# Optimization experiments

Hardware: AMD Instinct MI355X
Metric: run time of the kernel (lower is better)

## Reference

```python
import jax, jax.numpy as jnp
import numpy as np

INF = 10000000000000.0
HEADS = 12
HEAD_SIZE = 64

def _rope_tables(seqlen, dim):
    inv_freq = 1.0 / (10000.0 ** (jnp.arange(0, dim, 2, dtype=jnp.float32) / dim))
    t = jnp.arange(seqlen, dtype=jnp.float32)
    freqs = t[:, None] * inv_freq[None, :]            # [S, d/2]
    # unsqueeze_dim=-2 -> [S, 1, d/2] to broadcast over heads
    return jnp.sin(freqs)[:, None, :], jnp.cos(freqs)[:, None, :]

def _apply_rope(t, sin, cos):
    # t: [B, S, H, D]; sin/cos: [S, 1, D/2]
    t1, t2 = t[..., 0::2], t[..., 1::2]
    out = jnp.stack([t1 * cos - t2 * sin, t1 * sin + t2 * cos], axis=-1)
    return out.reshape(t.shape)

def setup_inputs() -> dict:
    key = jax.random.key(0)
    k1, k2 = jax.random.split(key)
    B, S, Hd = 32, 512, 1024
    x = jax.random.normal(k1, (B, S, Hd), dtype=jnp.float32)
    W = jax.random.normal(k2, (Hd, HEADS * 2 * HEAD_SIZE), dtype=jnp.float32) * (1.0 / np.sqrt(Hd))
    b = jnp.zeros((HEADS * 2 * HEAD_SIZE,), dtype=jnp.float32)
    attention_mask = jnp.ones((B, S), dtype=jnp.int32)
    return {"x": x, "W": W, "b": b, "attention_mask": attention_mask}

def reference(x, W, b, attention_mask):
    B, S, _ = x.shape
    proj = x @ W + b                                   # [B, S, H*2*D]
    proj = proj.reshape(B, S, HEADS, 2, HEAD_SIZE)
    qw, kw = proj[..., 0, :], proj[..., 1, :]          # [B, S, H, D]
    sin, cos = _rope_tables(S, HEAD_SIZE)
    qw = _apply_rope(qw, sin, cos)
    kw = _apply_rope(kw, sin, cos)
    logits = jnp.einsum('bmhd,bnhd->bhmn', qw, kw)     # [B, H, S, S]
    am = attention_mask.astype(logits.dtype)
    pad_mask = 1.0 - am[:, None, None, :] * am[:, None, :, None]
    logits = logits - pad_mask * INF
    idx = jnp.arange(S)
    tril = (idx[:, None] > idx[None, :]).astype(logits.dtype)  # strictly lower triangle
    logits = logits - tril * INF
    return logits / (HEAD_SIZE ** 0.5)
```

## Files before the change

kernel.cpp:

```cpp
#include <hip/hip_runtime.h>
#include <hip/hip_bf16.h>
#include <cstdint>

#define HEADS 12
#define HEAD_SIZE 64
#define SEQ 512
#define HD 1024
#define NPROJ 1536
#define INF_VAL 1e13f

typedef __attribute__((ext_vector_type(8))) __bf16 bf16x8;
typedef __attribute__((ext_vector_type(4))) float f32x4;

__device__ __forceinline__ unsigned short f2bf(float f) {
    unsigned u = __float_as_uint(f);
    u += 0x7fffu + ((u >> 16) & 1u);
    return (unsigned short)(u >> 16);
}

__device__ __forceinline__ void gl_lds16(const unsigned short* g, unsigned short* l) {
    __builtin_amdgcn_global_load_lds(
        (const __attribute__((address_space(1))) unsigned int*)g,
        (__attribute__((address_space(3))) unsigned int*)l, 16, 0, 0);
}

__global__ void __launch_bounds__(256) convert_x(const float* __restrict__ x,
                                                 unsigned short* __restrict__ xb) {
    const int i = blockIdx.x * 256 + threadIdx.x;
    const float4* src = (const float4*)x;
    float4 v0 = src[i * 2 + 0];
    float4 v1 = src[i * 2 + 1];
    uint4 p;
    p.x = f2bf(v0.x) | ((unsigned)f2bf(v0.y) << 16);
    p.y = f2bf(v0.z) | ((unsigned)f2bf(v0.w) << 16);
    p.z = f2bf(v1.x) | ((unsigned)f2bf(v1.y) << 16);
    p.w = f2bf(v1.z) | ((unsigned)f2bf(v1.w) << 16);
    ((uint4*)xb)[i] = p;
}

__global__ void __launch_bounds__(256) transpose_cast_w(const float* __restrict__ W,
                                                        unsigned short* __restrict__ Wt) {
    __shared__ unsigned short tile[64][65];
    const int bx = blockIdx.x;
    const int k0 = (bx & 15) * 64;
    const int n0 = (bx >> 4) * 64;
    const int t = threadIdx.x;
    const int tr = t >> 4;
    const int tc = (t & 15) * 4;
#pragma unroll
    for (int i = 0; i < 4; ++i) {
        int kk = tr + i * 16;
        float4 v = *(const float4*)&W[(size_t)(k0 + kk) * NPROJ + n0 + tc];
        tile[kk][tc + 0] = f2bf(v.x);
        tile[kk][tc + 1] = f2bf(v.y);
        tile[kk][tc + 2] = f2bf(v.z);
        tile[kk][tc + 3] = f2bf(v.w);
    }
    __syncthreads();
#pragma unroll
    for (int i = 0; i < 4; ++i) {
        int nn = tr + i * 16;
        ushort4 o;
        o.x = tile[tc + 0][nn];
        o.y = tile[tc + 1][nn];
        o.z = tile[tc + 2][nn];
        o.w = tile[tc + 3][nn];
        *(ushort4*)&Wt[(size_t)(n0 + nn) * HD + k0 + tc] = o;
    }
}

__global__ void __launch_bounds__(256) gemm1_rope(const unsigned short* __restrict__ xb,
                                                  const unsigned short* __restrict__ Wt,
                                                  const float* __restrict__ bias,
                                                  unsigned short* __restrict__ qws,
                                                  unsigned short* __restrict__ kws) {
    __shared__ __align__(16) char smem[32768];
    unsigned short* Alds = (unsigned short*)smem;
    unsigned short* Blds = (unsigned short*)(smem + 8192);

    const int bx = blockIdx.x;
    const int tile_m = bx / HEADS;
    const int h = bx - tile_m * HEADS;
    const int m0 = tile_m * 128;
    const int n0 = h * 128;

    const int t = threadIdx.x;
    const int w = t >> 6;
    const int lane = t & 63;
    const int wm = w >> 1;
    const int wn = w & 1;
    const int c16 = lane & 15;
    const int quad = lane >> 4;

    const int row0 = w * 32 + (lane >> 2);
    const int celem = (lane & 3) * 8;
    const unsigned short* ga0 = xb + (size_t)(m0 + row0) * HD + celem;
    const unsigned short* ga1 = xb + (size_t)(m0 + row0 + 16) * HD + celem;
    const unsigned short* gb0 = Wt + (size_t)(n0 + row0) * HD + celem;
    const unsigned short* gb1 = Wt + (size_t)(n0 + row0 + 16) * HD + celem;
    unsigned short* la0 = Alds + row0 * 32 + celem;
    unsigned short* la1 = Alds + (row0 + 16) * 32 + celem;
    unsigned short* lb0 = Blds + row0 * 32 + celem;
    unsigned short* lb1 = Blds + (row0 + 16) * 32 + celem;

    f32x4 acc[4][4];
#pragma unroll
    for (int i = 0; i < 4; ++i)
#pragma unroll
        for (int j = 0; j < 4; ++j) acc[i][j] = (f32x4){0.f, 0.f, 0.f, 0.f};

    for (int kt = 0; kt < HD; kt += 32) {
        gl_lds16(ga0 + kt, la0);
        gl_lds16(ga1 + kt, la1);
        gl_lds16(gb0 + kt, lb0);
        gl_lds16(gb1 + kt, lb1);
        __syncthreads();

        bf16x8 af[4], bfr[4];
#pragma unroll
        for (int mi = 0; mi < 4; ++mi)
            af[mi] = *(const bf16x8*)((char*)Alds + (wm * 64 + mi * 16 + c16) * 64 + quad * 16);
#pragma unroll
        for (int ni = 0; ni < 4; ++ni)
            bfr[ni] = *(const bf16x8*)((char*)Blds + (wn * 64 + ni * 16 + c16) * 64 + quad * 16);
#pragma unroll
        for (int mi = 0; mi < 4; ++mi)
#pragma unroll
            for (int ni = 0; ni < 4; ++ni)
                acc[mi][ni] = __builtin_amdgcn_mfma_f32_16x16x32_bf16(af[mi], bfr[ni], acc[mi][ni], 0, 0, 0);
        __syncthreads();
    }

    float bv[4];
#pragma unroll
    for (int ni = 0; ni < 4; ++ni) bv[ni] = bias[n0 + wn * 64 + ni * 16 + c16];

    float2* tab = (float2*)smem;
    const int sbase = m0 & (SEQ - 1);
#pragma unroll
    for (int i = 0; i < 16; ++i) {
        int e = t * 16 + i;
        int srow = e >> 5;
        int fi = e & 31;
        float invf = __expf(-(float)fi * (0.03125f * 9.210340371976184f));
        float theta = (float)(sbase + srow) * invf;
        float sv, cv;
        __sincosf(theta, &sv, &cv);
        tab[e] = make_float2(sv, cv);
    }
    __syncthreads();

    unsigned short* outp = wn ? kws : qws;
#pragma unroll
    for (int mi = 0; mi < 4; ++mi) {
#pragma unroll
        for (int ni = 0; ni < 4; ++ni) {
            int d = ni * 16 + c16;
            int fi = d >> 1;
            float sgn = (d & 1) ? 1.f : -1.f;
#pragma unroll
            for (int r = 0; r < 4; ++r) {
                float v = acc[mi][ni][r] + bv[ni];
                float p = __shfl_xor(v, 1, 64);
                int srow = wm * 64 + mi * 16 + quad * 4 + r;
                float2 sc2 = tab[srow * 32 + fi];
                float o = v * sc2.y + sgn * p * sc2.x;
                int m = m0 + srow;
                int bb = m >> 9;
                int ss = m & (SEQ - 1);
                outp[((size_t)(bb * HEADS + h) * SEQ + ss) * HEAD_SIZE + d] = f2bf(o);
            }
        }
    }
}

__global__ void __launch_bounds__(256) gemm2_mask(const unsigned short* __restrict__ qws,
                                                  const unsigned short* __restrict__ kws,
                                                  const int* __restrict__ am,
                                                  float* __restrict__ out) {
    __shared__ __align__(16) unsigned short qlds[128 * 72];
    __shared__ __align__(16) unsigned short klds[128 * 72];
    const int bh = blockIdx.y;
    const int b = bh / HEADS;
    const int tm = (blockIdx.x >> 2) * 128;
    const int tn = (blockIdx.x & 3) * 128;
    const int t = threadIdx.x;
    const int w = t >> 6, lane = t & 63;
    const int wm = w >> 1, wn = w & 1;
    const int c16 = lane & 15, quad = lane >> 4;

    {
        const int sr = t >> 1;
        const int sc = (t & 1) * 32;
        const uint4* src = (const uint4*)(qws + ((size_t)bh * SEQ + tm + sr) * HEAD_SIZE + sc);
        uint4* dst = (uint4*)((char*)qlds + sr * 144 + sc * 2);
        dst[0] = src[0]; dst[1] = src[1]; dst[2] = src[2]; dst[3] = src[3];
        const uint4* src2 = (const uint4*)(kws + ((size_t)bh * SEQ + tn + sr) * HEAD_SIZE + sc);
        uint4* dst2 = (uint4*)((char*)klds + sr * 144 + sc * 2);
        dst2[0] = src2[0]; dst2[1] = src2[1]; dst2[2] = src2[2]; dst2[3] = src2[3];
    }
    __syncthreads();

    f32x4 acc[4][4];
#pragma unroll
    for (int i = 0; i < 4; ++i)
#pragma unroll
        for (int j = 0; j < 4; ++j) acc[i][j] = (f32x4){0.f, 0.f, 0.f, 0.f};

#pragma unroll
    for (int ks = 0; ks < 2; ++ks) {
        bf16x8 af[4], bfr[4];
#pragma unroll
        for (int mi = 0; mi < 4; ++mi)
            af[mi] = *(const bf16x8*)((char*)qlds + (wm * 64 + mi * 16 + c16) * 144 + ks * 64 + quad * 16);
#pragma unroll
        for (int ni = 0; ni < 4; ++ni)
            bfr[ni] = *(const bf16x8*)((char*)klds + (wn * 64 + ni * 16 + c16) * 144 + ks * 64 + quad * 16);
#pragma unroll
        for (int mi = 0; mi < 4; ++mi)
#pragma unroll
            for (int ni = 0; ni < 4; ++ni)
                acc[mi][ni] = __builtin_amdgcn_mfma_f32_16x16x32_bf16(af[mi], bfr[ni], acc[mi][ni], 0, 0, 0);
    }

    const int* amb = am + b * SEQ;
    float amn[4];
#pragma unroll
    for (int ni = 0; ni < 4; ++ni) amn[ni] = (float)amb[tn + wn * 64 + ni * 16 + c16];
#pragma unroll
    for (int mi = 0; mi < 4; ++mi) {
#pragma unroll
        for (int r = 0; r < 4; ++r) {
            int m = tm + wm * 64 + mi * 16 + quad * 4 + r;
            float amm = (float)amb[m];
#pragma unroll
            for (int ni = 0; ni < 4; ++ni) {
                int n = tn + wn * 64 + ni * 16 + c16;
                float pen = (1.0f - amm * amn[ni]) + ((m > n) ? 1.0f : 0.0f);
                out[((size_t)bh * SEQ + m) * SEQ + n] = (acc[mi][ni][r] - pen * INF_VAL) * 0.125f;
            }
        }
    }
}

extern "C" void kernel_launch(void* const* d_in, const int* in_sizes, int n_in,
                              void* d_out, int out_size, void* d_ws, size_t ws_size,
                              hipStream_t stream) {
    (void)in_sizes; (void)n_in; (void)out_size; (void)ws_size;
    const float* x = (const float*)d_in[0];
    const float* W = (const float*)d_in[1];
    const float* bias = (const float*)d_in[2];
    const int* am = (const int*)d_in[3];
    float* out = (float*)d_out;

    unsigned short* Wt  = (unsigned short*)d_ws;
    unsigned short* qws = (unsigned short*)((char*)d_ws + 3145728);
    unsigned short* kws = (unsigned short*)((char*)d_ws + 3145728 + 25165824);
    unsigned short* xb  = (unsigned short*)((char*)d_ws + 3145728 + 2 * 25165824);

    hipLaunchKernelGGL(convert_x, dim3(8192), dim3(256), 0, stream, x, xb);
    hipLaunchKernelGGL(transpose_cast_w, dim3(384), dim3(256), 0, stream, W, Wt);
    hipLaunchKernelGGL(gemm1_rope, dim3(128 * HEADS), dim3(256), 0, stream, xb, Wt, bias, qws, kws);
    hipLaunchKernelGGL(gemm2_mask, dim3(16, 32 * HEADS), dim3(256), 0, stream, qws, kws, am, out);
}
```

Before: 547.9 us.

## Precompute RoPE table, stage gemm1 output via LDS, vectorize masked logits stores

Adds a small kernel that builds the sin/cos RoPE table once in workspace, so gemm1 no longer recomputes it in every block. gemm1 now packs bf16 pairs, stages the rotated Q/K tiles in swizzled LDS, and writes them back with coalesced 16-byte stores. gemm2 swaps the MFMA operands so each lane holds four consecutive columns, which allows float4 stores of the masked, scaled logits and int4 mask loads. The cost is an extra kernel launch and more LDS per gemm1 block. The output write in gemm2, which dominates traffic, should coalesce better.

```diff
diff --git a/kernel.cpp b/kernel.cpp
--- a/kernel.cpp
+++ b/kernel.cpp
@@ -69,12 +69,24 @@
     }
 }
 
+__global__ void __launch_bounds__(256) rope_table(float2* __restrict__ tab) {
+    const int e = blockIdx.x * 256 + threadIdx.x;
+    const int srow = e >> 5;
+    const int fi = e & 31;
+    float invf = __expf(-(float)fi * (0.03125f * 9.210340371976184f));
+    float theta = (float)srow * invf;
+    float sv, cv;
+    __sincosf(theta, &sv, &cv);
+    tab[e] = make_float2(sv, cv);
+}
+
 __global__ void __launch_bounds__(256) gemm1_rope(const unsigned short* __restrict__ xb,
                                                   const unsigned short* __restrict__ Wt,
                                                   const float* __restrict__ bias,
+                                                  const float2* __restrict__ tab,
                                                   unsigned short* __restrict__ qws,
                                                   unsigned short* __restrict__ kws) {
-    __shared__ __align__(16) char smem[32768];
+    __shared__ __align__(16) char smem[36864];
     unsigned short* Alds = (unsigned short*)smem;
     unsigned short* Blds = (unsigned short*)(smem + 8192);
 
@@ -135,42 +147,50 @@
 #pragma unroll
     for (int ni = 0; ni < 4; ++ni) bv[ni] = bias[n0 + wn * 64 + ni * 16 + c16];
 
-    float2* tab = (float2*)smem;
+    const int bb = m0 >> 9;
     const int sbase = m0 & (SEQ - 1);
-#pragma unroll
-    for (int i = 0; i < 16; ++i) {
-        int e = t * 16 + i;
-        int srow = e >> 5;
-        int fi = e & 31;
-        float invf = __expf(-(float)fi * (0.03125f * 9.210340371976184f));
-        float theta = (float)(sbase + srow) * invf;
-        float sv, cv;
-        __sincosf(theta, &sv, &cv);
-        tab[e] = make_float2(sv, cv);
-    }
-    __syncthreads();
-
-    unsigned short* outp = wn ? kws : qws;
+    const float2* tb = tab + sbase * 32;
+    char* stage = smem + wn * 18432;
+    const int odd = lane & 1;
+
 #pragma unroll
     for (int mi = 0; mi < 4; ++mi) {
 #pragma unroll
         for (int ni = 0; ni < 4; ++ni) {
-            int d = ni * 16 + c16;
-            int fi = d >> 1;
-            float sgn = (d & 1) ? 1.f : -1.f;
+            const int d = ni * 16 + c16;
+            const int fi = d >> 1;
 #pragma unroll
             for (int r = 0; r < 4; ++r) {
+                const int srow = wm * 64 + mi * 16 + quad * 4 + r;
                 float v = acc[mi][ni][r] + bv[ni];
                 float p = __shfl_xor(v, 1, 64);
-                int srow = wm * 64 + mi * 16 + quad * 4 + r;
-                float2 sc2 = tab[srow * 32 + fi];
-                float o = v * sc2.y + sgn * p * sc2.x;
-                int m = m0 + srow;
-                int bb = m >> 9;
-                int ss = m & (SEQ - 1);
-                outp[((size_t)(bb * HEADS + h) * SEQ + ss) * HEAD_SIZE + d] = f2bf(o);
+                float ve = odd ? p : v;
+                float vo = odd ? v : p;
+                float2 sc = tb[srow * 32 + fi];
+                float oe = ve * sc.y - vo * sc.x;
+                float oo = vo * sc.y + ve * sc.x;
+                unsigned pk;
+                asm("v_cvt_pk_bf16_f32 %0, %1, %2" : "=v"(pk) : "v"(oe), "v"(oo));
+                if (!odd) {
+                    int boff = srow * 144 + ((fi * 4) ^ ((srow & 7) << 4));
+                    *(unsigned*)(stage + boff) = pk;
+                }
             }
         }
+    }
+    __syncthreads();
+
+    const size_t gq = ((size_t)(bb * HEADS + h) * SEQ + sbase) * HEAD_SIZE;
+#pragma unroll
+    for (int it = 0; it < 8; ++it) {
+        int chunk = it * 256 + t;
+        int tile = chunk >> 10;
+        int c = chunk & 1023;
+        int row = c >> 3;
+        int cc = c & 7;
+        uint4 v = *(const uint4*)(smem + tile * 18432 + row * 144 + ((cc * 16) ^ ((row & 7) << 4)));
+        unsigned short* dstb = tile ? kws : qws;
+        *(uint4*)&dstb[gq + row * 64 + cc * 8] = v;
     }
 }
 
@@ -220,25 +240,29 @@
         for (int mi = 0; mi < 4; ++mi)
 #pragma unroll
             for (int ni = 0; ni < 4; ++ni)
-                acc[mi][ni] = __builtin_amdgcn_mfma_f32_16x16x32_bf16(af[mi], bfr[ni], acc[mi][ni], 0, 0, 0);
+                acc[mi][ni] = __builtin_amdgcn_mfma_f32_16x16x32_bf16(bfr[ni], af[mi], acc[mi][ni], 0, 0, 0);
     }
 
     const int* amb = am + b * SEQ;
-    float amn[4];
-#pragma unroll
-    for (int ni = 0; ni < 4; ++ni) amn[ni] = (float)amb[tn + wn * 64 + ni * 16 + c16];
-#pragma unroll
-    for (int mi = 0; mi < 4; ++mi) {
-#pragma unroll
-        for (int r = 0; r < 4; ++r) {
-            int m = tm + wm * 64 + mi * 16 + quad * 4 + r;
-            float amm = (float)amb[m];
-#pragma unroll
-            for (int ni = 0; ni < 4; ++ni) {
-                int n = tn + wn * 64 + ni * 16 + c16;
-                float pen = (1.0f - amm * amn[ni]) + ((m > n) ? 1.0f : 0.0f);
-                out[((size_t)bh * SEQ + m) * SEQ + n] = (acc[mi][ni][r] - pen * INF_VAL) * 0.125f;
-            }
+    float ammv[4];
+#pragma unroll
+    for (int mi = 0; mi < 4; ++mi) ammv[mi] = (float)amb[tm + wm * 64 + mi * 16 + c16];
+
+#pragma unroll
+    for (int ni = 0; ni < 4; ++ni) {
+        const int nb = tn + wn * 64 + ni * 16 + quad * 4;
+        const int4 a4 = *(const int4*)&amb[nb];
+        const float an0 = (float)a4.x, an1 = (float)a4.y, an2 = (float)a4.z, an3 = (float)a4.w;
+#pragma unroll
+        for (int mi = 0; mi < 4; ++mi) {
+            const int m = tm + wm * 64 + mi * 16 + c16;
+            const float amm = ammv[mi];
+            float4 o;
+            o.x = (acc[mi][ni][0] - ((1.0f - amm * an0) + ((m > nb + 0) ? 1.0f : 0.0f)) * INF_VAL) * 0.125f;
+            o.y = (acc[mi][ni][1] - ((1.0f - amm * an1) + ((m > nb + 1) ? 1.0f : 0.0f)) * INF_VAL) * 0.125f;
+            o.z = (acc[mi][ni][2] - ((1.0f - amm * an2) + ((m > nb + 2) ? 1.0f : 0.0f)) * INF_VAL) * 0.125f;
+            o.w = (acc[mi][ni][3] - ((1.0f - amm * an3) + ((m > nb + 3) ? 1.0f : 0.0f)) * INF_VAL) * 0.125f;
+            *(float4*)&out[((size_t)bh * SEQ + m) * SEQ + nb] = o;
         }
     }
 }
@@ -257,9 +281,11 @@
     unsigned short* qws = (unsigned short*)((char*)d_ws + 3145728);
     unsigned short* kws = (unsigned short*)((char*)d_ws + 3145728 + 25165824);
     unsigned short* xb  = (unsigned short*)((char*)d_ws + 3145728 + 2 * 25165824);
+    float2* tab = (float2*)((char*)d_ws + 3145728 + 2 * 25165824 + 33554432);
 
     hipLaunchKernelGGL(convert_x, dim3(8192), dim3(256), 0, stream, x, xb);
     hipLaunchKernelGGL(transpose_cast_w, dim3(384), dim3(256), 0, stream, W, Wt);
-    hipLaunchKernelGGL(gemm1_rope, dim3(128 * HEADS), dim3(256), 0, stream, xb, Wt, bias, qws, kws);
+    hipLaunchKernelGGL(rope_table, dim3(64), dim3(256), 0, stream, tab);
+    hipLaunchKernelGGL(gemm1_rope, dim3(128 * HEADS), dim3(256), 0, stream, xb, Wt, bias, tab, qws, kws);
     hipLaunchKernelGGL(gemm2_mask, dim3(16, 32 * HEADS), dim3(256), 0, stream, qws, kws, am, out);
 }
```

New measurement: 585.7 us. 6.9% more time.
